# Performance work log

Hardware: AMD Instinct MI355X
Metric: run time of the kernel (lower is better)

Reference implementation:

```python
import jax, jax.numpy as jnp
import numpy as np

ROPE_BASE = 10000.0

def _rope(x, positions):
    # x: [B, H, T, hs], rotate-half (GPT-NeoX style) rotary embedding
    hs = x.shape[-1]
    half = hs // 2
    inv_freq = 1.0 / (ROPE_BASE ** (jnp.arange(half, dtype=jnp.float32) / half))
    ang = positions.astype(jnp.float32)[:, None] * inv_freq[None, :]  # [T, half]
    cos, sin = jnp.cos(ang), jnp.sin(ang)
    x1, x2 = x[..., :half], x[..., half:]
    return jnp.concatenate([x1 * cos - x2 * sin, x1 * sin + x2 * cos], axis=-1)


def setup_inputs() -> dict:
    key = jax.random.key(0)
    ks = jax.random.split(key, 8)
    B, T, OFF, C, H = 1, 1024, 1024, 2048, 16
    hs = C // H
    return {
        "x": jax.random.normal(ks[0], (B, T, C), jnp.float32),
        "cached_k": jax.random.normal(ks[1], (B, H, OFF, hs), jnp.float32),
        "cached_v": jax.random.normal(ks[2], (B, H, OFF, hs), jnp.float32),
        "W_attn": jax.random.normal(ks[3], (C, 3 * C), jnp.float32) * 0.02,
        "b_attn": jnp.zeros((3 * C,), jnp.float32),
        "W_proj": jax.random.normal(ks[4], (C, C), jnp.float32) * 0.02,
        "b_proj": jnp.zeros((C,), jnp.float32),
        "decay_raw": jax.random.normal(ks[5], (16,), jnp.float32) * 0.5,
    }


def reference(x, cached_k, cached_v, W_attn, b_attn, W_proj, b_proj, decay_raw):
    B, T, C = x.shape
    H = decay_raw.shape[0]
    hs = C // H
    off = cached_k.shape[2]

    qkv = x @ W_attn + b_attn                       # [B, T, 3C]
    q, k, v = jnp.split(qkv, 3, axis=-1)
    to_heads = lambda t: t.reshape(B, T, H, hs).transpose(0, 2, 1, 3)  # [B,H,T,hs]
    q, k, v = to_heads(q), to_heads(k), to_heads(v)

    positions = jnp.arange(off, off + T)
    q = _rope(q, positions)
    k = _rope(k, positions)

    k = jnp.concatenate([cached_k, k], axis=2)      # [B, H, T_full, hs]
    v = jnp.concatenate([cached_v, v], axis=2)
    T_full = k.shape[2]

    # causal mask over full key length, offset for cache
    neg_inf = jnp.finfo(jnp.float32).min
    q_idx = positions                               # [T]
    k_idx = jnp.arange(T_full)                      # [T_full]
    causal = jnp.where(k_idx[None, :] > q_idx[:, None], neg_inf, 0.0)  # [T, T_full]

    # per-head distance-decay log-bias
    decay = jax.nn.softplus(decay_raw)              # [H]
    dist = jnp.maximum(q_idx[:, None] - k_idx[None, :], 0).astype(jnp.float32)
    logw = -jnp.log1p(decay[:, None, None] * jnp.log1p(dist))          # [H, T, T_full]
    bias = causal[None, :, :] + logw                # [H, T, T_full]

    scale = 1.0 / jnp.sqrt(jnp.float32(hs))
    scores = jnp.einsum('bhtd,bhsd->bhts', q, k) * scale + bias[None]
    attn = jax.nn.softmax(scores, axis=-1)
    y = jnp.einsum('bhts,bhsd->bhtd', attn, v)      # [B, H, T, hs]
    y = y.transpose(0, 2, 1, 3).reshape(B, T, C)
    y = y @ W_proj + b_proj
    return (y, k, v)
```

## Files before the change

### kernel.cpp

```cpp
#include <hip/hip_runtime.h>
#include <hip/hip_bf16.h>

typedef unsigned short u16;
typedef unsigned int u32;
typedef __attribute__((ext_vector_type(4))) float f32x4;
typedef float f32x4u __attribute__((ext_vector_type(4), aligned(4)));
typedef __attribute__((ext_vector_type(8))) short bf16x8;

__device__ __forceinline__ u16 f2bf(float f) {
    union { float f; u32 u; } v; v.f = f;
    return (u16)((v.u + 0x7FFFu + ((v.u >> 16) & 1u)) >> 16);
}
__device__ __forceinline__ float bf2f(u16 b) {
    union { u32 u; float f; } v; v.u = ((u32)b) << 16;
    return v.f;
}
__device__ __forceinline__ void st_out(float* p, float v) { *p = v; }
__device__ __forceinline__ void st_out(u16* p, float v) { *p = f2bf(v); }

__device__ __forceinline__ f32x4 mfma16(bf16x8 a, bf16x8 b, f32x4 c) {
    return __builtin_amdgcn_mfma_f32_16x16x32_bf16(a, b, c, 0, 0, 0);
}
__device__ __forceinline__ u32 cvt_pk_bf16(float lo, float hi) {
    u32 r;
    asm("v_cvt_pk_bf16_f32 %0, %1, %2" : "=v"(r) : "v"(lo), "v"(hi));
    return r;
}
template<int N> __device__ __forceinline__ void wait_vmcnt() {
    if constexpr (N == 0) asm volatile("s_waitcnt vmcnt(0)" ::: "memory");
    else if constexpr (N == 2) asm volatile("s_waitcnt vmcnt(2)" ::: "memory");
    else if constexpr (N == 3) asm volatile("s_waitcnt vmcnt(3)" ::: "memory");
    else if constexpr (N == 4) asm volatile("s_waitcnt vmcnt(4)" ::: "memory");
    else if constexpr (N == 6) asm volatile("s_waitcnt vmcnt(6)" ::: "memory");
    else if constexpr (N == 7) asm volatile("s_waitcnt vmcnt(7)" ::: "memory");
}

#define GLD_LDS16(g, l) __builtin_amdgcn_global_load_lds( \
    (const __attribute__((address_space(1))) void*)(g),   \
    (__attribute__((address_space(3))) void*)(l), 16, 0, 0)

#define LOG2E 1.4426950408889634f
#define QSCALE 0.12751743f

__global__ __launch_bounds__(256) void k_prep(
    const float* __restrict__ W_attn, const float* __restrict__ W_proj,
    const float* __restrict__ x, const float* __restrict__ decay_raw,
    u16* __restrict__ WaT, u16* __restrict__ WpT, u16* __restrict__ Xb,
    float* __restrict__ bias_tab, float* __restrict__ cosT, float* __restrict__ sinT) {
    __shared__ float tile[64][65];
    const int b = blockIdx.x, tid = threadIdx.x;
    if (b < 4096) {
        const float* src; u16* dst; int R, Cc, bx, by;
        if (b < 3072) { src = W_attn; dst = WaT; R = 2048; Cc = 6144; bx = b % 96; by = b / 96; }
        else          { src = W_proj; dst = WpT; R = 2048; Cc = 2048; bx = (b - 3072) & 31; by = (b - 3072) >> 5; }
        int c0 = bx * 64, r0 = by * 64;
#pragma unroll
        for (int it = 0; it < 16; ++it) {
            int idx = it * 256 + tid;
            int r = idx >> 6, c = idx & 63;
            tile[r][c] = src[(size_t)(r0 + r) * Cc + c0 + c];
        }
        __syncthreads();
#pragma unroll
        for (int it = 0; it < 16; ++it) {
            int idx = it * 256 + tid;
            int cc = idx >> 6, rr = idx & 63;
            dst[(size_t)(c0 + cc) * R + r0 + rr] = f2bf(tile[rr][cc]);
        }
    } else if (b < 6144) {
        int i = (b - 4096) * 256 + tid;
        float4 v = ((const float4*)x)[i];
        u32 p0 = (u32)f2bf(v.x) | ((u32)f2bf(v.y) << 16);
        u32 p1 = (u32)f2bf(v.z) | ((u32)f2bf(v.w) << 16);
        uint2 p; p.x = p0; p.y = p1;
        *(uint2*)(Xb + (size_t)i * 4) = p;
    } else {
        int i = (b - 6144) * 256 + tid;
        if (i < 16 * 2048) {
            int h = i >> 11, dist = i & 2047;
            float dec = log1pf(expf(decay_raw[h]));
            bias_tab[i] = -log1pf(dec * log1pf((float)dist)) * LOG2E;
        }
        if (i < 1024 * 64) {
            int t = i >> 6, j = i & 63;
            float inv = expf(-logf(10000.0f) * (float)j / 64.0f);
            float ang = (float)(1024 + t) * inv;
            cosT[i] = cosf(ang);
            sinT[i] = sinf(ang);
        }
    }
}

template<int BM, int BN, int WRG, int WCG, typename OT>
__global__ __launch_bounds__(256) void k_gemm_bt(
    const u16* __restrict__ A, const u16* __restrict__ Bt,
    const float* __restrict__ bias, OT* __restrict__ C,
    int M, int N, int K) {
    constexpr int BK = 64;
    constexpr int WM = BM / WRG;
    constexpr int WN = BN / WCG;
    constexpr int MR = WM / 16;
    constexpr int NR = WN / 16;
    constexpr int LDSZ = (BM + BN) * BK * 2;
    constexpr int NLOAD = (BM + BN) * 8 / 256;
    __shared__ char lds[2][LDSZ];

    const int tid = threadIdx.x;
    const int lane = tid & 63, wid = tid >> 6;
    const int wr = wid / WCG, wc = wid % WCG;
    const int lhi = lane >> 4, llo = lane & 15;
    const int m0 = blockIdx.y * BM, n0 = blockIdx.x * BN;

    f32x4 acc[MR][NR];
#pragma unroll
    for (int m = 0; m < MR; ++m)
#pragma unroll
        for (int n = 0; n < NR; ++n)
            acc[m][n] = f32x4{0.f, 0.f, 0.f, 0.f};

    auto stage = [&](int buf, int k0) {
        char* ldsA = &lds[buf][0];
        char* ldsB = &lds[buf][0] + BM * BK * 2;
#pragma unroll
        for (int it = 0; it < (BM * 8) / 256; ++it) {
            int ci = it * 256 + wid * 64 + lane;
            int r = ci >> 3, c = ci & 7;
            int sc = c ^ (r & 7);
            GLD_LDS16(A + (size_t)(m0 + r) * K + k0 + sc * 8,
                      ldsA + (it * 256 + wid * 64) * 16);
        }
#pragma unroll
        for (int it = 0; it < (BN * 8) / 256; ++it) {
            int ci = it * 256 + wid * 64 + lane;
            int r = ci >> 3, c = ci & 7;
            int sc = c ^ (r & 7);
            GLD_LDS16(Bt + (size_t)(n0 + r) * K + k0 + sc * 8,
                      ldsB + (it * 256 + wid * 64) * 16);
        }
    };

    stage(0, 0);
    int cur = 0;
    for (int k0 = 0; k0 < K; k0 += BK) {
        if (k0 + BK < K) {
            stage(cur ^ 1, k0 + BK);
            wait_vmcnt<NLOAD>();
        } else {
            wait_vmcnt<0>();
        }
        __builtin_amdgcn_s_barrier();
        __builtin_amdgcn_sched_barrier(0);
        asm volatile("" ::: "memory");
        const char* ldsA = &lds[cur][0];
        const char* ldsB = &lds[cur][0] + BM * BK * 2;
#pragma unroll
        for (int kk = 0; kk < BK; kk += 32) {
            bf16x8 af[MR], bfr[NR];
            const int clb = (kk >> 3) + lhi;
#pragma unroll
            for (int m = 0; m < MR; ++m) {
                int row = wr * WM + m * 16 + llo;
                af[m] = *(const bf16x8*)(ldsA + row * 128 + ((clb ^ (row & 7)) << 4));
            }
#pragma unroll
            for (int n = 0; n < NR; ++n) {
                int row = wc * WN + n * 16 + llo;
                bfr[n] = *(const bf16x8*)(ldsB + row * 128 + ((clb ^ (row & 7)) << 4));
            }
#pragma unroll
            for (int m = 0; m < MR; ++m)
#pragma unroll
                for (int n = 0; n < NR; ++n)
                    acc[m][n] = mfma16(af[m], bfr[n], acc[m][n]);
        }
        asm volatile("" ::: "memory");
        __builtin_amdgcn_sched_barrier(0);
        __builtin_amdgcn_s_barrier();
        __builtin_amdgcn_sched_barrier(0);
        asm volatile("" ::: "memory");
        cur ^= 1;
    }
#pragma unroll
    for (int m = 0; m < MR; ++m) {
        int row = m0 + wr * WM + m * 16 + lhi * 4;
#pragma unroll
        for (int n = 0; n < NR; ++n) {
            int col = n0 + wc * WN + n * 16 + llo;
            float bv = bias[col];
#pragma unroll
            for (int j = 0; j < 4; ++j)
                st_out(&C[(size_t)(row + j) * N + col], acc[m][n][j] + bv);
        }
    }
}

__global__ __launch_bounds__(256) void k_mid(
    const u16* __restrict__ qkv,
    const float* __restrict__ cosT, const float* __restrict__ sinT,
    const float* __restrict__ cached_k, const float* __restrict__ cached_v,
    u16* __restrict__ qb, u16* __restrict__ kb,
    float* __restrict__ out_k, float* __restrict__ out_v, u16* __restrict__ vt) {
    __shared__ u16 tile[64][65];
    const int b = blockIdx.x;
    if (b < 4096) {
        int i = b * 256 + threadIdx.x;
        int j = i & 63;
        int t = (i >> 6) & 1023;
        int h = i >> 16;
        const u16* row = qkv + (size_t)t * 6144;
        float q1 = bf2f(row[h * 128 + j]),        q2 = bf2f(row[h * 128 + j + 64]);
        float k1 = bf2f(row[2048 + h * 128 + j]), k2 = bf2f(row[2048 + h * 128 + j + 64]);
        float cv = cosT[t * 64 + j], sv = sinT[t * 64 + j];
        float qo1 = q1 * cv - q2 * sv, qo2 = q1 * sv + q2 * cv;
        float ko1 = k1 * cv - k2 * sv, ko2 = k1 * sv + k2 * cv;
        size_t qoff = ((size_t)h * 1024 + t) * 128 + j;
        qb[qoff] = f2bf(qo1 * QSCALE); qb[qoff + 64] = f2bf(qo2 * QSCALE);
        size_t koff = ((size_t)h * 2048 + 1024 + t) * 128 + j;
        kb[koff] = f2bf(ko1); kb[koff + 64] = f2bf(ko2);
        out_k[koff] = ko1; out_k[koff + 64] = ko2;
    } else if (b < 12288) {
        int i = (b - 4096) * 256 + threadIdx.x;
        int d = i & 127, s = (i >> 7) & 1023, h = i >> 17;
        float v = cached_k[i];
        size_t off = ((size_t)h * 2048 + s) * 128 + d;
        out_k[off] = v;
        kb[off] = f2bf(v);
    } else {
        int idx2 = b - 12288;
        int s0 = (idx2 & 31) * 64, d0 = ((idx2 >> 5) & 1) * 64, h = idx2 >> 6;
        int tid = threadIdx.x;
#pragma unroll
        for (int it = 0; it < 16; ++it) {
            int idx = it * 256 + tid;
            int r = idx >> 6, c = idx & 63;
            int s = s0 + r, d = d0 + c;
            u16 v = (s < 1024)
                ? f2bf(cached_v[((size_t)h * 1024 + s) * 128 + d])
                : qkv[(size_t)(s - 1024) * 6144 + 4096 + h * 128 + d];
            tile[r][c] = v;
            out_v[((size_t)h * 2048 + s) * 128 + d] = bf2f(v);
        }
        __syncthreads();
#pragma unroll
        for (int it = 0; it < 16; ++it) {
            int idx = it * 256 + tid;
            int dd = idx >> 6, ss = idx & 63;
            vt[((size_t)h * 128 + d0 + dd) * 2048 + s0 + ss] = tile[ss][dd];
        }
    }
}

__global__ __launch_bounds__(256, 4) void k_attn(
    const u16* __restrict__ qb,
    const u16* __restrict__ kb,
    const u16* __restrict__ vt,
    const float* __restrict__ bias_tab,
    u16* __restrict__ Pacc,
    float* __restrict__ Pm,
    float* __restrict__ Pl) {
    __shared__ char ldsK[2][32 * 256];
    __shared__ char ldsV[2][128 * 64];

    const int bid = blockIdx.x;
    const int xcd = bid & 7, idx = bid >> 3;
    const int work = xcd * 128 + idx;
    const int h = work >> 6, rem = work & 63;
    const int qt = 15 - (rem >> 2), chunk = rem & 3;
    const int qbase = qt * 64;
    const int tid = threadIdx.x, lane = tid & 63, wid = tid >> 6;
    const int lhi = lane >> 4, llo = lane & 15;
    const int slot = (h * 16 + qt) * 4 + chunk;

    const u16* kg = kb + (size_t)h * 2048 * 128;
    const u16* vg = vt + (size_t)h * 128 * 2048;
    const float* bt = bias_tab + h * 2048;

    bf16x8 qf[4];
    {
        const u16* qrow = qb + ((size_t)h * 1024 + qbase + wid * 16 + llo) * 128;
#pragma unroll
        for (int c = 0; c < 4; ++c)
            qf[c] = *(const bf16x8*)(qrow + c * 32 + lhi * 8);
    }

    f32x4 acc[8];
#pragma unroll
    for (int d = 0; d < 8; ++d) acc[d] = f32x4{0.f, 0.f, 0.f, 0.f};
    float mrow = -3e38f;
    float lrow = 0.f;

    const int ntiles = 34 + 2 * qt;
    const int qpos = 1024 + qbase + wid * 16 + llo;

    auto stage = [&](int b, int st) {
        int sbase = st * 32;
#pragma unroll
        for (int it = 0; it < 2; ++it) {
            int ci = it * 256 + tid;
            int r = ci >> 4, c = ci & 15;
            int sc = c ^ (r & 7);
            GLD_LDS16(kg + (size_t)(sbase + r) * 128 + sc * 8,
                      &ldsK[b][0] + (it * 256 + wid * 64) * 16);
        }
#pragma unroll
        for (int it = 0; it < 2; ++it) {
            int ci = it * 256 + tid;
            int r = ci >> 2, c = ci & 3;
            int sc = c ^ ((r >> 1) & 3);
            GLD_LDS16(vg + (size_t)r * 2048 + sbase + sc * 8,
                      &ldsV[b][0] + (it * 256 + wid * 64) * 16);
        }
    };

    auto permP = [&](u32 p0, u32 p1, u32 p2, u32 p3) -> bf16x8 {
        u32 r16a = (u32)__shfl_xor((int)(lhi == 1 ? p0 : p2), 16);
        u32 r16b = (u32)__shfl_xor((int)(lhi == 1 ? p1 : p3), 16);
        u32 r32a = (u32)__shfl_xor((int)(lhi == 3 ? p0 : p2), 32);
        u32 r32b = (u32)__shfl_xor((int)(lhi == 3 ? p1 : p3), 32);
        u32 r48a = (u32)__shfl_xor((int)(lhi == 2 ? p0 : p2), 48);
        u32 r48b = (u32)__shfl_xor((int)(lhi == 2 ? p1 : p3), 48);
        union { u32 w[4]; bf16x8 v; } u;
        u.w[0] = lhi == 0 ? p0 : lhi == 1 ? r48a : lhi == 2 ? r32a : r16a;
        u.w[1] = lhi == 0 ? p1 : lhi == 1 ? r48b : lhi == 2 ? r32b : r16b;
        u.w[2] = lhi == 0 ? r16a : lhi == 1 ? r32a : lhi == 2 ? r48a : p2;
        u.w[3] = lhi == 0 ? r16b : lhi == 1 ? r32b : lhi == 2 ? r48b : p3;
        return u.v;
    };

    const int st0 = chunk + 4 * ((ntiles - 1 - chunk) >> 2);
    stage(0, st0);
    __syncthreads();
    int cur = 0;
    for (int st = st0; st >= chunk; st -= 4) {
        if (st >= chunk + 4) stage(cur ^ 1, st - 4);
        const int sbase = st * 32;
        const char* lK = &ldsK[cur][0];
        const char* lV = &ldsV[cur][0];

        const int D0 = qpos - sbase - lhi * 4;
        f32x4u wB = *(const f32x4u*)(bt + (D0 - 3 < 0 ? 0 : D0 - 3));
        f32x4u wC = *(const f32x4u*)(bt + (D0 - 19 < 0 ? 0 : D0 - 19));

        f32x4 sc4[2];
        __builtin_amdgcn_s_setprio(1);
#pragma unroll
        for (int sub = 0; sub < 2; ++sub) {
            f32x4 s4 = f32x4{0.f, 0.f, 0.f, 0.f};
            int key = sub * 16 + llo;
#pragma unroll
            for (int c2 = 0; c2 < 4; ++c2) {
                int cl = c2 * 4 + lhi;
                bf16x8 kf = *(const bf16x8*)(lK + key * 256 + ((cl ^ (key & 7)) << 4));
                s4 = mfma16(kf, qf[c2], s4);
            }
            sc4[sub] = s4;
        }
        __builtin_amdgcn_s_setprio(0);

        if (sbase + 31 <= 1024 + qbase + wid * 16) {
#pragma unroll
            for (int j = 0; j < 4; ++j) {
                sc4[0][j] += wB[3 - j];
                sc4[1][j] += wC[3 - j];
            }
        } else {
#pragma unroll
            for (int sub = 0; sub < 2; ++sub)
#pragma unroll
                for (int j = 0; j < 4; ++j) {
                    int key = sbase + sub * 16 + lhi * 4 + j;
                    int dist = qpos - key;
                    float bv = bt[dist < 0 ? 0 : dist];
                    sc4[sub][j] = (dist < 0) ? -3e38f : sc4[sub][j] + bv;
                }
        }

        float tmax = fmaxf(fmaxf(fmaxf(sc4[0][0], sc4[0][1]), fmaxf(sc4[0][2], sc4[0][3])),
                           fmaxf(fmaxf(sc4[1][0], sc4[1][1]), fmaxf(sc4[1][2], sc4[1][3])));
        int ok = (tmax <= mrow + 8.0f) ? 1 : 0;
        if (!__all(ok)) {
            float t = tmax;
            t = fmaxf(t, __shfl_xor(t, 16));
            t = fmaxf(t, __shfl_xor(t, 32));
            float mnew = fmaxf(mrow, t);
            float fs = exp2f(mrow - mnew);
            mrow = mnew;
            lrow *= fs;
            float fsj[4];
#pragma unroll
            for (int j = 0; j < 4; ++j)
                fsj[j] = __shfl(fs, lhi * 4 + j);
#pragma unroll
            for (int d = 0; d < 8; ++d)
#pragma unroll
                for (int j = 0; j < 4; ++j) acc[d][j] *= fsj[j];
        }

        float p[8];
#pragma unroll
        for (int sub = 0; sub < 2; ++sub)
#pragma unroll
            for (int j = 0; j < 4; ++j)
                p[sub * 4 + j] = exp2f(sc4[sub][j] - mrow);
        u32 pk0 = cvt_pk_bf16(p[0], p[1]), pk1 = cvt_pk_bf16(p[2], p[3]);
        u32 pk2 = cvt_pk_bf16(p[4], p[5]), pk3 = cvt_pk_bf16(p[6], p[7]);
        lrow += bf2f((u16)(pk0 & 0xFFFF)) + bf2f((u16)(pk0 >> 16))
              + bf2f((u16)(pk1 & 0xFFFF)) + bf2f((u16)(pk1 >> 16))
              + bf2f((u16)(pk2 & 0xFFFF)) + bf2f((u16)(pk2 >> 16))
              + bf2f((u16)(pk3 & 0xFFFF)) + bf2f((u16)(pk3 >> 16));
        bf16x8 pa = permP(pk0, pk1, pk2, pk3);

        __builtin_amdgcn_s_setprio(1);
#pragma unroll
        for (int db = 0; db < 8; ++db) {
            int dr = db * 16 + llo;
            int cl = lhi ^ ((dr >> 1) & 3);
            bf16x8 vf = *(const bf16x8*)(lV + dr * 64 + cl * 16);
            acc[db] = mfma16(pa, vf, acc[db]);
        }
        __builtin_amdgcn_s_setprio(0);
        __syncthreads();
        cur ^= 1;
    }

    {
        float t = lrow;
        t += __shfl_xor(t, 16);
        t += __shfl_xor(t, 32);
        lrow = t;
    }

    if (lhi == 0) {
        int r = wid * 16 + llo;
        Pm[(size_t)slot * 64 + r] = mrow;
        Pl[(size_t)slot * 64 + r] = lrow;
    }
#pragma unroll
    for (int db = 0; db < 8; ++db)
#pragma unroll
        for (int j = 0; j < 4; ++j) {
            int r = wid * 16 + lhi * 4 + j;
            Pacc[(size_t)slot * 8192 + r * 128 + db * 16 + llo] = f2bf(acc[db][j]);
        }
}

__global__ __launch_bounds__(256) void k_merge(
    const u16* __restrict__ Pacc, const float* __restrict__ Pm,
    const float* __restrict__ Pl, u16* __restrict__ yb) {
    const int b = blockIdx.x;
    const int h = b >> 6, qt = (b >> 2) & 15, quarter = b & 3;
    const int slot0 = (h * 16 + qt) * 4;
    const int tid = threadIdx.x;
    const int r = tid >> 2, dd = (tid & 3) * 8 + quarter * 32;

    float m[4], l[4];
#pragma unroll
    for (int c = 0; c < 4; ++c) {
        m[c] = Pm[(size_t)(slot0 + c) * 64 + r];
        l[c] = Pl[(size_t)(slot0 + c) * 64 + r];
    }
    float M = fmaxf(fmaxf(m[0], m[1]), fmaxf(m[2], m[3]));
    float w[4], L = 0.f;
#pragma unroll
    for (int c = 0; c < 4; ++c) {
        w[c] = exp2f(m[c] - M);
        L += w[c] * l[c];
    }
    float inv = 1.0f / L;

    float y[8];
#pragma unroll
    for (int i = 0; i < 8; ++i) y[i] = 0.f;
#pragma unroll
    for (int c = 0; c < 4; ++c) {
        const uint4* pa = (const uint4*)(Pacc + (size_t)(slot0 + c) * 8192 + r * 128 + dd);
        float wc = w[c];
        uint4 v = *pa;
        u32 a[4] = {v.x, v.y, v.z, v.w};
#pragma unroll
        for (int p = 0; p < 4; ++p) {
            y[p * 2]     += wc * bf2f((u16)(a[p] & 0xFFFF));
            y[p * 2 + 1] += wc * bf2f((u16)(a[p] >> 16));
        }
    }
    int trow = qt * 64 + r;
    uint4 outv;
    u32* ow = (u32*)&outv;
#pragma unroll
    for (int k = 0; k < 4; ++k)
        ow[k] = (u32)f2bf(y[2 * k] * inv) | ((u32)f2bf(y[2 * k + 1] * inv) << 16);
    *(uint4*)(yb + (size_t)trow * 2048 + h * 128 + dd) = outv;
}

extern "C" void kernel_launch(void* const* d_in, const int* in_sizes, int n_in,
                              void* d_out, int out_size, void* d_ws, size_t ws_size,
                              hipStream_t stream) {
    (void)in_sizes; (void)n_in; (void)out_size;
    const float* x         = (const float*)d_in[0];
    const float* cached_k  = (const float*)d_in[1];
    const float* cached_v  = (const float*)d_in[2];
    const float* W_attn    = (const float*)d_in[3];
    const float* b_attn    = (const float*)d_in[4];
    const float* W_proj    = (const float*)d_in[5];
    const float* b_proj    = (const float*)d_in[6];
    const float* decay_raw = (const float*)d_in[7];

    float* out_y = (float*)d_out;
    float* out_k = out_y + 2097152;
    float* out_v = out_y + 6291456;

    char* ws = (char*)d_ws;
    if (ws_size < 63569920) return;
    u16*   WaT  = (u16*)(ws);
    u16*   WpT  = (u16*)(ws + 25165824);
    u16*   Xb   = (u16*)(ws + 33554432);
    u16*   QKVb = (u16*)(ws + 37748736);
    float* BT   = (float*)(ws + 62914560);
    float* CT   = (float*)(ws + 63045632);
    float* ST   = (float*)(ws + 63307776);
    u16*   Qb   = (u16*)(ws);
    u16*   Kb   = (u16*)(ws + 4194304);
    u16*   Vt   = (u16*)(ws + 12582912);
    u16*   Yb   = (u16*)(ws + 20971520);
    float* Pm   = (float*)(ws + 33554432);
    float* Pl   = (float*)(ws + 33816576);
    u16*   Pacc = (u16*)(ws + 37748736);

    k_prep<<<6400, 256, 0, stream>>>(W_attn, W_proj, x, decay_raw, WaT, WpT, Xb, BT, CT, ST);
    k_gemm_bt<128, 64, 2, 2, u16><<<dim3(96, 8), 256, 0, stream>>>(Xb, WaT, b_attn, QKVb, 1024, 6144, 2048);
    k_mid<<<13312, 256, 0, stream>>>(QKVb, CT, ST, cached_k, cached_v, Qb, Kb, out_k, out_v, Vt);
    k_attn<<<1024, 256, 0, stream>>>(Qb, Kb, Vt, BT, Pacc, Pm, Pl);
    k_merge<<<1024, 256, 0, stream>>>(Pacc, Pm, Pl, Yb);
    k_gemm_bt<64, 32, 2, 2, float><<<dim3(64, 16), 256, 0, stream>>>(Yb, WpT, b_proj, out_y, 1024, 2048, 2048);
}
```

Measured before the change: 135.0 us.

## Vectorize transpose stores, remap GEMM blocks per XCD, simplify GEMM pipeline sync

The weight and V transposes now pack four bf16 values into one 8-byte store instead of writing scalar u16, which cuts store instruction count. The GEMM switches to a 1D grid remapped so that consecutive tiles land on the same XCD, sharing columns of B in that XCD's L2. It also swaps the hand-tuned vmcnt waits and sched barriers for plain __syncthreads. That is simpler, but the compiler may now insert a full vmcnt(0) wait and lose the overlap between prefetch and MFMA.

New measurement: 133.0 us. Within noise of the previous version (-1.4%).

```diff
diff --git a/kernel.cpp b/kernel.cpp
--- a/kernel.cpp
+++ b/kernel.cpp
@@ -25,14 +25,6 @@
     u32 r;
     asm("v_cvt_pk_bf16_f32 %0, %1, %2" : "=v"(r) : "v"(lo), "v"(hi));
     return r;
-}
-template<int N> __device__ __forceinline__ void wait_vmcnt() {
-    if constexpr (N == 0) asm volatile("s_waitcnt vmcnt(0)" ::: "memory");
-    else if constexpr (N == 2) asm volatile("s_waitcnt vmcnt(2)" ::: "memory");
-    else if constexpr (N == 3) asm volatile("s_waitcnt vmcnt(3)" ::: "memory");
-    else if constexpr (N == 4) asm volatile("s_waitcnt vmcnt(4)" ::: "memory");
-    else if constexpr (N == 6) asm volatile("s_waitcnt vmcnt(6)" ::: "memory");
-    else if constexpr (N == 7) asm volatile("s_waitcnt vmcnt(7)" ::: "memory");
 }
 
 #define GLD_LDS16(g, l) __builtin_amdgcn_global_load_lds( \
@@ -62,10 +54,14 @@
         }
         __syncthreads();
 #pragma unroll
-        for (int it = 0; it < 16; ++it) {
+        for (int it = 0; it < 4; ++it) {
             int idx = it * 256 + tid;
-            int cc = idx >> 6, rr = idx & 63;
-            dst[(size_t)(c0 + cc) * R + r0 + rr] = f2bf(tile[rr][cc]);
+            int cc = idx >> 4;
+            int rr0 = (idx & 15) * 4;
+            u32 lo = (u32)f2bf(tile[rr0][cc])     | ((u32)f2bf(tile[rr0 + 1][cc]) << 16);
+            u32 hi = (u32)f2bf(tile[rr0 + 2][cc]) | ((u32)f2bf(tile[rr0 + 3][cc]) << 16);
+            uint2 p; p.x = lo; p.y = hi;
+            *(uint2*)(dst + (size_t)(c0 + cc) * R + r0 + rr0) = p;
         }
     } else if (b < 6144) {
         int i = (b - 4096) * 256 + tid;
@@ -102,14 +98,17 @@
     constexpr int MR = WM / 16;
     constexpr int NR = WN / 16;
     constexpr int LDSZ = (BM + BN) * BK * 2;
-    constexpr int NLOAD = (BM + BN) * 8 / 256;
     __shared__ char lds[2][LDSZ];
 
     const int tid = threadIdx.x;
     const int lane = tid & 63, wid = tid >> 6;
     const int wr = wid / WCG, wc = wid % WCG;
     const int lhi = lane >> 4, llo = lane & 15;
-    const int m0 = blockIdx.y * BM, n0 = blockIdx.x * BN;
+
+    const int per = gridDim.x >> 3;
+    const int w = (blockIdx.x & 7) * per + (blockIdx.x >> 3);
+    const int mblocks = M / BM;
+    const int m0 = (w % mblocks) * BM, n0 = (w / mblocks) * BN;
 
     f32x4 acc[MR][NR];
 #pragma unroll
@@ -140,17 +139,10 @@
     };
 
     stage(0, 0);
+    __syncthreads();
     int cur = 0;
     for (int k0 = 0; k0 < K; k0 += BK) {
-        if (k0 + BK < K) {
-            stage(cur ^ 1, k0 + BK);
-            wait_vmcnt<NLOAD>();
-        } else {
-            wait_vmcnt<0>();
-        }
-        __builtin_amdgcn_s_barrier();
-        __builtin_amdgcn_sched_barrier(0);
-        asm volatile("" ::: "memory");
+        if (k0 + BK < K) stage(cur ^ 1, k0 + BK);
         const char* ldsA = &lds[cur][0];
         const char* ldsB = &lds[cur][0] + BM * BK * 2;
 #pragma unroll
@@ -173,11 +165,7 @@
                 for (int n = 0; n < NR; ++n)
                     acc[m][n] = mfma16(af[m], bfr[n], acc[m][n]);
         }
-        asm volatile("" ::: "memory");
-        __builtin_amdgcn_sched_barrier(0);
-        __builtin_amdgcn_s_barrier();
-        __builtin_amdgcn_sched_barrier(0);
-        asm volatile("" ::: "memory");
+        __syncthreads();
         cur ^= 1;
     }
 #pragma unroll
@@ -242,10 +230,14 @@
         }
         __syncthreads();
 #pragma unroll
-        for (int it = 0; it < 16; ++it) {
+        for (int it = 0; it < 4; ++it) {
             int idx = it * 256 + tid;
-            int dd = idx >> 6, ss = idx & 63;
-            vt[((size_t)h * 128 + d0 + dd) * 2048 + s0 + ss] = tile[ss][dd];
+            int dd = idx >> 4;
+            int ss0 = (idx & 15) * 4;
+            u32 lo = (u32)tile[ss0][dd]     | ((u32)tile[ss0 + 1][dd] << 16);
+            u32 hi = (u32)tile[ss0 + 2][dd] | ((u32)tile[ss0 + 3][dd] << 16);
+            uint2 p; p.x = lo; p.y = hi;
+            *(uint2*)(vt + ((size_t)h * 128 + d0 + dd) * 2048 + s0 + ss0) = p;
         }
     }
 }
@@ -527,9 +519,9 @@
     u16*   Pacc = (u16*)(ws + 37748736);
 
     k_prep<<<6400, 256, 0, stream>>>(W_attn, W_proj, x, decay_raw, WaT, WpT, Xb, BT, CT, ST);
-    k_gemm_bt<128, 64, 2, 2, u16><<<dim3(96, 8), 256, 0, stream>>>(Xb, WaT, b_attn, QKVb, 1024, 6144, 2048);
+    k_gemm_bt<128, 64, 2, 2, u16><<<768, 256, 0, stream>>>(Xb, WaT, b_attn, QKVb, 1024, 6144, 2048);
     k_mid<<<13312, 256, 0, stream>>>(QKVb, CT, ST, cached_k, cached_v, Qb, Kb, out_k, out_v, Vt);
     k_attn<<<1024, 256, 0, stream>>>(Qb, Kb, Vt, BT, Pacc, Pm, Pl);
     k_merge<<<1024, 256, 0, stream>>>(Pacc, Pm, Pl, Yb);
-    k_gemm_bt<64, 32, 2, 2, float><<<dim3(64, 16), 256, 0, stream>>>(Yb, WpT, b_proj, out_y, 1024, 2048, 2048);
-}
+    k_gemm_bt<64, 32, 2, 2, float><<<1024, 256, 0, stream>>>(Yb, WpT, b_proj, out_y, 1024, 2048, 2048);
+}
```
